# Optimization experiments

Measured on AMD Instinct MI355X. Metric: run time of the kernel, lower is better.

Reference implementation:

```python
import jax, jax.numpy as jnp
import numpy as np

N, T, F, H = 64, 256, 1024, 1024

def setup_inputs() -> dict:
    key = jax.random.key(0)
    k1, k2 = jax.random.split(key)
    x = jax.random.normal(k1, (N, T, F), dtype=jnp.float32)
    # xavier-normal: std = sqrt(2 / (fan_in + fan_out))
    std = np.sqrt(2.0 / ((F + H) + 4 * H)).astype(np.float32)
    weight = jax.random.normal(k2, (F + H, 4 * H), dtype=jnp.float32) * std
    bias = jnp.zeros((1, 4 * H), dtype=jnp.float32)
    return {"x": x, "weight": weight, "bias": bias}


def reference(x, weight, bias):
    # x: [N, T, F]; weight: [F+H, 4H]; bias: [1, 4H]
    n, t, f = x.shape
    h_dim = weight.shape[1] // 4

    def step(carry, xt):
        h, mem = carry  # [N, H] each
        xh = jnp.concatenate([xt, h], axis=-1)          # [N, F+H]
        a = xh @ weight + bias                          # [N, 4H]
        i, fg, o, g = jnp.split(a, 4, axis=-1)
        mem = jax.nn.sigmoid(fg) * mem + jax.nn.sigmoid(i) * jnp.tanh(g)
        h = jax.nn.sigmoid(o) * jnp.tanh(mem)
        return (h, mem), h

    h0 = jnp.zeros((n, h_dim), dtype=x.dtype)
    m0 = jnp.zeros((n, h_dim), dtype=x.dtype)
    (h, mem), z_tnh = jax.lax.scan(step, (h0, m0), jnp.swapaxes(x, 0, 1))
    z = jnp.swapaxes(z_tnh, 0, 1)                       # [N, T, H]
    return z, h, mem
```

## Files before the change

### kernel.cpp

```cpp
#include <hip/hip_runtime.h>

typedef unsigned short u16;
typedef unsigned int   u32;
typedef __attribute__((ext_vector_type(8))) short bf16x8;
typedef __attribute__((ext_vector_type(4))) float f32x4;

#define NB 64
#define TT 256
#define FF 1024
#define HH 1024
#define KK 2048
#define GG 4096
#define NBLK 256

#define WPACK_SZ  (KK*GG)
#define XPACK_SZ  ((size_t)NB*TT*FF)
#define HPACK_SZ  (2*4*32*64*8)
#define FLAGS_SZ  (4*64*4)

__device__ __forceinline__ u16 f2bf(float f) {
  u32 u = __float_as_uint(f);
  u32 r = (u + 0x7FFFu + ((u >> 16) & 1u)) >> 16;
  return (u16)r;
}

__global__ void pack_w(const float* __restrict__ W, u16* __restrict__ wp) {
  int tid = blockIdx.x * blockDim.x + threadIdx.x;
  if (tid >= (KK * GG / 16)) return;
  int j  = tid & 7;
  int g  = (tid >> 3) & 3;
  int kt = (tid >> 5) & 63;
  int ct = tid >> 11;
  int k  = kt * 32 + g * 8 + j;
  const float* src = W + (size_t)k * GG + ct * 16;
  u16* dst = wp + (size_t)(ct * 64 + kt) * 512 + j;
  float4 v0 = *(const float4*)(src + 0);
  float4 v1 = *(const float4*)(src + 4);
  float4 v2 = *(const float4*)(src + 8);
  float4 v3 = *(const float4*)(src + 12);
  float vv[16] = {v0.x,v0.y,v0.z,v0.w, v1.x,v1.y,v1.z,v1.w,
                  v2.x,v2.y,v2.z,v2.w, v3.x,v3.y,v3.z,v3.w};
  #pragma unroll
  for (int c = 0; c < 16; ++c) dst[(size_t)(g * 16 + c) * 8] = f2bf(vv[c]);
}

__global__ void pack_x(const float* __restrict__ X, u16* __restrict__ xp) {
  int tid = blockIdx.x * blockDim.x + threadIdx.x;
  if (tid >= (int)(NB * TT * FF / 8)) return;
  int l  = tid & 63;
  int kt = (tid >> 6) & 31;
  int rt = (tid >> 11) & 3;
  int t  = tid >> 13;
  int n  = rt * 16 + (l & 15);
  int f  = kt * 32 + (l >> 4) * 8;
  const float* src = X + (size_t)n * TT * FF + (size_t)t * FF + f;
  float4 a = *(const float4*)(src);
  float4 b = *(const float4*)(src + 4);
  u16 tmp[8] = { f2bf(a.x), f2bf(a.y), f2bf(a.z), f2bf(a.w),
                 f2bf(b.x), f2bf(b.y), f2bf(b.z), f2bf(b.w) };
  *(uint4*)(xp + (size_t)((t * 4 + rt) * 32 + kt) * 512 + l * 8) = *(uint4*)tmp;
}

__global__ void init_state(u32* __restrict__ flags) {
  int tid = threadIdx.x;
  #pragma unroll
  for (int i = 0; i < 4; ++i)
    __hip_atomic_store(&flags[i * 256 + tid], 0u, __ATOMIC_RELAXED,
                       __HIP_MEMORY_SCOPE_AGENT);
}

__launch_bounds__(1024, 1)
__global__ void lstm_main(const u16* __restrict__ wp, const u16* __restrict__ xp,
                          u32* __restrict__ hp32, const float* __restrict__ bias,
                          float* __restrict__ z, float* __restrict__ hout,
                          float* __restrict__ memout, u32* flags) {
  const int b   = blockIdx.x;
  const int cgi = b & 63;
  const int rt  = b >> 6;
  const int tid = threadIdx.x;
  const int w16 = tid >> 6;
  const int g   = w16 & 3;
  const int s   = w16 >> 2;
  const int l   = tid & 63;
  const int ct  = g * 64 + cgi;

  const u16* bp = wp + (size_t)ct * 32768 + l * 8;
  const float bv = (s == 0) ? bias[ct * 16 + (l & 15)] : 0.f;
  u32* gf = flags + rt * 256;

  __shared__ __align__(16) u16 whl[49152];
  __shared__ u32   hs32[8192];
  __shared__ float gl[4][4][16][16];

  #pragma unroll
  for (int j = 0; j < 6; ++j) {
    int byte = tid * 16 + j * 16384;
    int f    = byte >> 10;
    int ll   = (byte & 1023) >> 4;
    int gg   = f / 24, rem = f % 24;
    int s1   = rem >> 3, kt = rem & 7;
    const u16* src = wp + (size_t)(gg * 64 + cgi) * 32768
                        + (size_t)(32 + (s1 + 1) * 8 + kt) * 512 + ll * 8;
    *(uint4*)((char*)whl + byte) = *(const uint4*)src;
  }
  __syncthreads();

  const int er  = tid >> 4;
  const int ec  = tid & 15;
  const int m   = rt * 16 + er;
  const int col = cgi * 16 + ec;
  const int col0 = col & ~1;
  const int kt2  = col0 >> 5;
  const int g2   = (col0 >> 3) & 3;
  const int l2   = er | (g2 << 4);
  const int cbase = kt2 * 256 + l2 * 4 + ((col0 & 7) >> 1);

  float memv = 0.0f;

  for (int t = 0; t < TT; ++t) {
    const int p = t & 1;
    const u16* ax = xp + (size_t)((t * 4 + rt) * 32 + s * 8) * 512 + l * 8;
    const u16* bx = bp + (size_t)(s * 8) * 512;

    f32x4 acc0 = {bv, bv, bv, bv};
    f32x4 acc1 = {0.f, 0.f, 0.f, 0.f};
    #pragma unroll
    for (int kt = 0; kt < 8; kt += 2) {
      bf16x8 a0 = *(const bf16x8*)(ax + (size_t)kt * 512);
      bf16x8 b0 = *(const bf16x8*)(bx + (size_t)kt * 512);
      bf16x8 a1 = *(const bf16x8*)(ax + (size_t)(kt + 1) * 512);
      bf16x8 b1 = *(const bf16x8*)(bx + (size_t)(kt + 1) * 512);
      acc0 = __builtin_amdgcn_mfma_f32_16x16x32_bf16(a0, b0, acc0, 0, 0, 0);
      acc1 = __builtin_amdgcn_mfma_f32_16x16x32_bf16(a1, b1, acc1, 0, 0, 0);
    }

    if (t != 0) {
      const u32 tgt = (u32)t;
      for (;;) {
        u32 v = __hip_atomic_load(&gf[l * 4], __ATOMIC_RELAXED,
                                  __HIP_MEMORY_SCOPE_AGENT);
        if (l == cgi) v = tgt;
        if (!__any((int)(v < tgt))) break;
        __builtin_amdgcn_s_sleep(1);
      }

      const u32* hsrc = hp32 + (size_t)(p * 4 + rt) * 8192;
      u32 tmpv[8];
      #pragma unroll
      for (int i = 0; i < 8; ++i)
        tmpv[i] = __hip_atomic_load(hsrc + i * 1024 + tid, __ATOMIC_RELAXED,
                                    __HIP_MEMORY_SCOPE_AGENT);
      #pragma unroll
      for (int i = 0; i < 8; ++i)
        hs32[i * 1024 + tid] = tmpv[i];
      __syncthreads();

      const char* hb = (const char*)hs32 + (size_t)(s * 8) * 1024 + l * 16;
      if (s == 0) {
        const u16* bh = bp + (size_t)32 * 512;
        #pragma unroll
        for (int kt = 0; kt < 8; kt += 2) {
          bf16x8 a0 = *(const bf16x8*)(hb + (size_t)kt * 1024);
          bf16x8 b0 = *(const bf16x8*)(bh + (size_t)kt * 512);
          bf16x8 a1 = *(const bf16x8*)(hb + (size_t)(kt + 1) * 1024);
          bf16x8 b1 = *(const bf16x8*)(bh + (size_t)(kt + 1) * 512);
          acc0 = __builtin_amdgcn_mfma_f32_16x16x32_bf16(a0, b0, acc0, 0, 0, 0);
          acc1 = __builtin_amdgcn_mfma_f32_16x16x32_bf16(a1, b1, acc1, 0, 0, 0);
        }
      } else {
        const u16* bh = whl + (size_t)((g * 3 + (s - 1)) * 8) * 512 + l * 8;
        #pragma unroll
        for (int kt = 0; kt < 8; kt += 2) {
          bf16x8 a0 = *(const bf16x8*)(hb + (size_t)kt * 1024);
          bf16x8 b0 = *(const bf16x8*)(bh + (size_t)kt * 512);
          bf16x8 a1 = *(const bf16x8*)(hb + (size_t)(kt + 1) * 1024);
          bf16x8 b1 = *(const bf16x8*)(bh + (size_t)(kt + 1) * 512);
          acc0 = __builtin_amdgcn_mfma_f32_16x16x32_bf16(a0, b0, acc0, 0, 0, 0);
          acc1 = __builtin_amdgcn_mfma_f32_16x16x32_bf16(a1, b1, acc1, 0, 0, 0);
        }
      }
    }

    #pragma unroll
    for (int r = 0; r < 4; ++r)
      gl[s][g][(l >> 4) * 4 + r][l & 15] = acc0[r] + acc1[r];
    __syncthreads();

    float h;
    if (tid < 256) {
      float ai = (gl[0][0][er][ec] + gl[1][0][er][ec]) +
                 (gl[2][0][er][ec] + gl[3][0][er][ec]);
      float af = (gl[0][1][er][ec] + gl[1][1][er][ec]) +
                 (gl[2][1][er][ec] + gl[3][1][er][ec]);
      float ao = (gl[0][2][er][ec] + gl[1][2][er][ec]) +
                 (gl[2][2][er][ec] + gl[3][2][er][ec]);
      float ag = (gl[0][3][er][ec] + gl[1][3][er][ec]) +
                 (gl[2][3][er][ec] + gl[3][3][er][ec]);
      float si = 1.f / (1.f + __expf(-ai));
      float sf = 1.f / (1.f + __expf(-af));
      float so = 1.f / (1.f + __expf(-ao));
      float tg = 1.f - 2.f / (__expf(2.f * ag) + 1.f);
      memv = sf * memv + si * tg;
      float th = 1.f - 2.f / (__expf(2.f * memv) + 1.f);
      h = so * th;

      float hn = __shfl_xor(h, 1);
      if ((ec & 1) == 0) {
        u32 pair = (u32)f2bf(h) | ((u32)f2bf(hn) << 16);
        __hip_atomic_store(&hp32[(size_t)((p ^ 1) * 4 + rt) * 8192 + cbase], pair,
                           __ATOMIC_RELAXED, __HIP_MEMORY_SCOPE_AGENT);
      }
    }

    if (t < TT - 1) {
      __syncthreads();
      if (tid == 0)
        __hip_atomic_store(&gf[cgi * 4], (u32)(t + 1), __ATOMIC_RELAXED,
                           __HIP_MEMORY_SCOPE_AGENT);
    }

    if (tid < 256) {
      z[((size_t)m * TT + t) * HH + col] = h;
      if (t == TT - 1) hout[(size_t)m * HH + col] = h;
    }
  }
  if (tid < 256) memout[(size_t)m * HH + col] = memv;
}

extern "C" void kernel_launch(void* const* d_in, const int* in_sizes, int n_in,
                              void* d_out, int out_size, void* d_ws, size_t ws_size,
                              hipStream_t stream) {
  const float* x    = (const float*)d_in[0];
  const float* W    = (const float*)d_in[1];
  const float* bias = (const float*)d_in[2];

  float* z      = (float*)d_out;
  float* hout   = z + (size_t)NB * TT * HH;
  float* memout = hout + (size_t)NB * HH;

  u16* wp = (u16*)d_ws;
  u16* xp = wp + WPACK_SZ;
  u16* hp = xp + XPACK_SZ;
  u32* flags = (u32*)(hp + HPACK_SZ);

  hipLaunchKernelGGL(pack_w, dim3(2048), dim3(256), 0, stream, W, wp);
  hipLaunchKernelGGL(pack_x, dim3(8192), dim3(256), 0, stream, x, xp);
  hipLaunchKernelGGL(init_state, dim3(1), dim3(256), 0, stream, flags);

  hipLaunchKernelGGL(lstm_main, dim3(NBLK), dim3(1024), 0, stream,
                     wp, xp, (u32*)hp, bias, z, hout, memout, flags);
}
```

Measured before the change: 799.9 us.

## Prefetch next timestep's x tile into LDS and shrink LDS weight cache

The x operand for each timestep is now staged in shared memory. The next step's tile is loaded into registers during the current step and written to LDS after the gate reduction, so global x loads leave the critical path. To free LDS for that buffer, only two of the four recurrent-weight k-slices are cached in LDS; the other two waves now read their recurrent weights from global memory. This trades LDS capacity for more global weight traffic on the serial recurrent path.

Result: slower. 838.1 us (+4.8%).

```diff
diff --git a/kernel.cpp b/kernel.cpp
--- a/kernel.cpp
+++ b/kernel.cpp
@@ -88,20 +88,28 @@
   const float bv = (s == 0) ? bias[ct * 16 + (l & 15)] : 0.f;
   u32* gf = flags + rt * 256;
 
-  __shared__ __align__(16) u16 whl[49152];
+  __shared__ __align__(16) u16 whl[32768];
+  __shared__ u32   xs32[8192];
   __shared__ u32   hs32[8192];
   __shared__ float gl[4][4][16][16];
 
   #pragma unroll
-  for (int j = 0; j < 6; ++j) {
+  for (int j = 0; j < 4; ++j) {
     int byte = tid * 16 + j * 16384;
     int f    = byte >> 10;
     int ll   = (byte & 1023) >> 4;
-    int gg   = f / 24, rem = f % 24;
-    int s1   = rem >> 3, kt = rem & 7;
+    int gg   = f >> 4, rem = f & 15;
+    int s2   = rem >> 3, kt = rem & 7;
     const u16* src = wp + (size_t)(gg * 64 + cgi) * 32768
-                        + (size_t)(32 + (s1 + 1) * 8 + kt) * 512 + ll * 8;
+                        + (size_t)(48 + s2 * 8 + kt) * 512 + ll * 8;
     *(uint4*)((char*)whl + byte) = *(const uint4*)src;
+  }
+  {
+    const uint2* x0 = (const uint2*)(xp + (size_t)((0 * 4 + rt) * 32) * 512);
+    uint2* xd = (uint2*)xs32;
+    #pragma unroll
+    for (int i = 0; i < 4; ++i)
+      xd[i * 1024 + tid] = x0[i * 1024 + tid];
   }
   __syncthreads();
 
@@ -119,19 +127,28 @@
 
   for (int t = 0; t < TT; ++t) {
     const int p = t & 1;
-    const u16* ax = xp + (size_t)((t * 4 + rt) * 32 + s * 8) * 512 + l * 8;
-    const u16* bx = bp + (size_t)(s * 8) * 512;
-
+
+    const char* xb = (const char*)xs32 + (size_t)(s * 8) * 1024 + l * 16;
+    const u16*  bx = bp + (size_t)(s * 8) * 512;
     f32x4 acc0 = {bv, bv, bv, bv};
     f32x4 acc1 = {0.f, 0.f, 0.f, 0.f};
     #pragma unroll
     for (int kt = 0; kt < 8; kt += 2) {
-      bf16x8 a0 = *(const bf16x8*)(ax + (size_t)kt * 512);
+      bf16x8 a0 = *(const bf16x8*)(xb + (size_t)kt * 1024);
       bf16x8 b0 = *(const bf16x8*)(bx + (size_t)kt * 512);
-      bf16x8 a1 = *(const bf16x8*)(ax + (size_t)(kt + 1) * 512);
+      bf16x8 a1 = *(const bf16x8*)(xb + (size_t)(kt + 1) * 1024);
       bf16x8 b1 = *(const bf16x8*)(bx + (size_t)(kt + 1) * 512);
       acc0 = __builtin_amdgcn_mfma_f32_16x16x32_bf16(a0, b0, acc0, 0, 0, 0);
       acc1 = __builtin_amdgcn_mfma_f32_16x16x32_bf16(a1, b1, acc1, 0, 0, 0);
+    }
+
+    uint2 tx0, tx1, tx2, tx3;
+    if (t < TT - 1) {
+      const uint2* xn = (const uint2*)(xp + (size_t)(((t + 1) * 4 + rt) * 32) * 512);
+      tx0 = xn[0 * 1024 + tid];
+      tx1 = xn[1 * 1024 + tid];
+      tx2 = xn[2 * 1024 + tid];
+      tx3 = xn[3 * 1024 + tid];
     }
 
     if (t != 0) {
@@ -156,8 +173,8 @@
       __syncthreads();
 
       const char* hb = (const char*)hs32 + (size_t)(s * 8) * 1024 + l * 16;
-      if (s == 0) {
-        const u16* bh = bp + (size_t)32 * 512;
+      if (s < 2) {
+        const u16* bh = bp + (size_t)(32 + s * 8) * 512;
         #pragma unroll
         for (int kt = 0; kt < 8; kt += 2) {
           bf16x8 a0 = *(const bf16x8*)(hb + (size_t)kt * 1024);
@@ -168,7 +185,7 @@
           acc1 = __builtin_amdgcn_mfma_f32_16x16x32_bf16(a1, b1, acc1, 0, 0, 0);
         }
       } else {
-        const u16* bh = whl + (size_t)((g * 3 + (s - 1)) * 8) * 512 + l * 8;
+        const u16* bh = whl + (size_t)((g * 16 + (s - 2) * 8)) * 512 + l * 8;
         #pragma unroll
         for (int kt = 0; kt < 8; kt += 2) {
           bf16x8 a0 = *(const bf16x8*)(hb + (size_t)kt * 1024);
@@ -185,6 +202,14 @@
     for (int r = 0; r < 4; ++r)
       gl[s][g][(l >> 4) * 4 + r][l & 15] = acc0[r] + acc1[r];
     __syncthreads();
+
+    if (t < TT - 1) {
+      uint2* xd = (uint2*)xs32;
+      xd[0 * 1024 + tid] = tx0;
+      xd[1 * 1024 + tid] = tx1;
+      xd[2 * 1024 + tid] = tx2;
+      xd[3 * 1024 + tid] = tx3;
+    }
 
     float h;
     if (tid < 256) {
```
